# Performance work log

Hardware: AMD Instinct MI355X
Metric: run time of the kernel (lower is better)

The kernel has to match this reference:

```python
import jax, jax.numpy as jnp
import numpy as np

N = 50000      # total nodes
E = 500000     # edges
D = 128        # in_channels
B = 50         # graphs in batch
NPG = N // B   # nodes per graph (equal-sized graphs)
RATIO = 0.5
ALPHA = 0.6


def setup_inputs() -> dict:
    key = jax.random.key(0)
    ks = jax.random.split(key, 8)
    x = jax.random.normal(ks[0], (N, D), dtype=jnp.float32)
    edge_index = jax.random.randint(ks[1], (2, E), 0, N, dtype=jnp.int32)
    batch = jnp.repeat(jnp.arange(B, dtype=jnp.int32), NPG)  # sorted, equal blocks
    s = 1.0 / np.sqrt(D)
    # GCNConv(D,1) for structure score
    W_s = jax.random.normal(ks[2], (D, 1), dtype=jnp.float32) * s
    b_s = jnp.zeros((1,), dtype=jnp.float32)
    # Linear(D,1) for feature score
    W_f = jax.random.normal(ks[3], (1, D), dtype=jnp.float32) * s
    b_f = jnp.zeros((1,), dtype=jnp.float32)
    # GCNConv(D,D) fusion layer
    W_fu = jax.random.normal(ks[4], (D, D), dtype=jnp.float32) * s
    b_fu = jnp.zeros((D,), dtype=jnp.float32)
    return {"x": x, "edge_index": edge_index, "batch": batch,
            "W_s": W_s, "b_s": b_s, "W_f": W_f, "b_f": b_f,
            "W_fu": W_fu, "b_fu": b_fu}


def gcn_conv(x, src, dst, W, b, n):
    """PyG GCNConv: add self loops, symmetric D^-1/2 (A+I) D^-1/2 @ (xW) + b."""
    xw = x @ W                                  # [n, out]
    loop = jnp.arange(n, dtype=src.dtype)
    s = jnp.concatenate([src, loop])
    d = jnp.concatenate([dst, loop])
    deg = jax.ops.segment_sum(jnp.ones_like(s, dtype=xw.dtype), d, num_segments=n)
    dinv = jax.lax.rsqrt(jnp.maximum(deg, 1e-12))
    norm = dinv[s] * dinv[d]                    # [E+n]
    out = jax.ops.segment_sum(norm[:, None] * xw[s], d, num_segments=n)
    return out + b


def reference(x, edge_index, batch, W_s, b_s, W_f, b_f, W_fu, b_fu):
    src, dst = edge_index[0], edge_index[1]
    # fused score: alpha * structure (GCN) + (1-alpha) * feature (Linear)
    score_s = gcn_conv(x, src, dst, W_s, b_s, N)[:, 0]          # [N]
    score_f = (x @ W_f.T + b_f)[:, 0]                           # [N]
    score = jnp.tanh(ALPHA * score_s + (1.0 - ALPHA) * score_f)
    # per-graph top-k (equal-sized graphs -> dense [B, NPG] view, like the torch topk)
    k = int(np.ceil(RATIO * NPG))
    dense = score.reshape(B, NPG)
    order = jnp.argsort(-dense, axis=-1)                        # descending
    offsets = (jnp.arange(B, dtype=jnp.int32) * NPG)[:, None]
    perm = (order[:, :k].astype(jnp.int32) + offsets).reshape(-1)  # [B*k]
    # fusion conv on full graph, then gather selected nodes
    x_fused = gcn_conv(x, src, dst, W_fu, b_fu, N)              # [N, D]
    x_ae = x_fused[perm]                                        # [B*k, D]
    x_out = x_ae * score[perm][:, None]                         # multiplier == 1
    batch_out = batch[perm]
    # filter_adj: remap node ids, keep edges with both endpoints selected
    nodemap = jnp.full((N,), -1, dtype=jnp.int32).at[perm].set(
        jnp.arange(perm.shape[0], dtype=jnp.int32))
    r, c = nodemap[src], nodemap[dst]
    m = (r >= 0) & (c >= 0)
    edge_index_new = jnp.stack([r[m], c[m]], axis=0)
    return (x_out, edge_index_new, batch_out, perm, x_ae)
```

## Files before the change

kernel.cpp:

```cpp
#include <hip/hip_runtime.h>
#include <math.h>

#define N_NODES 50000
#define N_EDGES 500000
#define DIM     128
#define NGRAPH  50
#define NPGC    1000
#define KSEL    500
#define SORT_N  1024
#define NBE     489
#define GEMM_BLKS 782
#define EDGE_BLKS 1954
#define DOTS_BLKS 12500
#define NDINV     196
#define GATH_BLKS 6250
#define DEGB    64
#define NCHUNK  1954


__global__ __launch_bounds__(256) void k1_gemm_deg(const float* __restrict__ x,
                                                   const float* __restrict__ W,
                                                   float* __restrict__ xw,
                                                   const int* __restrict__ dst,
                                                   int* __restrict__ degpriv,
                                                   int* __restrict__ eslot) {
    __shared__ float lds[12288];
    int t = threadIdx.x;
    if (blockIdx.x < DEGB) {
        int b = blockIdx.x;
        int* priv = degpriv + b * N_NODES;
        for (int c = b; c < NCHUNK; c += 2 * DEGB) {
            int e1 = (c << 8) + t;
            int cB = c + DEGB;
            int e2 = (cB << 8) + t;
            int d1 = (e1 < N_EDGES) ? dst[e1] : -1;
            int d2 = (cB < NCHUNK && e2 < N_EDGES) ? dst[e2] : -1;
            if (d1 >= 0)
                eslot[e1] = __hip_atomic_fetch_add(&priv[d1], 1, __ATOMIC_RELAXED,
                                                   __HIP_MEMORY_SCOPE_WORKGROUP);
            if (d2 >= 0)
                eslot[e2] = __hip_atomic_fetch_add(&priv[d2], 1, __ATOMIC_RELAXED,
                                                   __HIP_MEMORY_SCOPE_WORKGROUP);
        }
        return;
    }
    float* Wt = lds;
    float* Xt = lds + 64 * DIM;
    int cg = t & 15;
    int ng = t >> 4;
    int node_base = (blockIdx.x - DEGB) * 64;

    float4 acc[4][2];
    #pragma unroll
    for (int nn = 0; nn < 4; nn++) {
        acc[nn][0] = make_float4(0.f, 0.f, 0.f, 0.f);
        acc[nn][1] = make_float4(0.f, 0.f, 0.f, 0.f);
    }
    for (int half = 0; half < 2; half++) {
        const float4* Wg = (const float4*)(W + half * 64 * DIM);
        float4* Wl = (float4*)Wt;
        #pragma unroll
        for (int i = 0; i < 8; i++) {
            int f = t + i * 256;
            Wl[f] = Wg[f];
        }
        #pragma unroll
        for (int i = 0; i < 4; i++) {
            int f = t + i * 256;
            int row = f >> 4, col = f & 15;
            int node = node_base + row;
            float4 v = make_float4(0.f, 0.f, 0.f, 0.f);
            if (node < N_NODES) v = *(const float4*)&x[(size_t)node * DIM + half * 64 + col * 4];
            *(float4*)&Xt[(row << 6) + ((col ^ (row & 15)) << 2)] = v;
        }
        __syncthreads();
        #pragma unroll 2
        for (int kc = 0; kc < 16; kc++) {
            int k = kc << 2;
            float4 wa[4], wb[4];
            #pragma unroll
            for (int kk = 0; kk < 4; kk++) {
                wa[kk] = *(const float4*)&Wt[(k + kk) * DIM + (cg << 2)];
                wb[kk] = *(const float4*)&Wt[(k + kk) * DIM + (cg << 2) + 64];
            }
            int csw = (kc ^ ng) << 2;
            #pragma unroll
            for (int nn = 0; nn < 4; nn++) {
                float4 xv = *(const float4*)&Xt[((ng + (nn << 4)) << 6) + csw];
                acc[nn][0].x += xv.x * wa[0].x + xv.y * wa[1].x + xv.z * wa[2].x + xv.w * wa[3].x;
                acc[nn][0].y += xv.x * wa[0].y + xv.y * wa[1].y + xv.z * wa[2].y + xv.w * wa[3].y;
                acc[nn][0].z += xv.x * wa[0].z + xv.y * wa[1].z + xv.z * wa[2].z + xv.w * wa[3].z;
                acc[nn][0].w += xv.x * wa[0].w + xv.y * wa[1].w + xv.z * wa[2].w + xv.w * wa[3].w;
                acc[nn][1].x += xv.x * wb[0].x + xv.y * wb[1].x + xv.z * wb[2].x + xv.w * wb[3].x;
                acc[nn][1].y += xv.x * wb[0].y + xv.y * wb[1].y + xv.z * wb[2].y + xv.w * wb[3].y;
                acc[nn][1].z += xv.x * wb[0].z + xv.y * wb[1].z + xv.z * wb[2].z + xv.w * wb[3].z;
                acc[nn][1].w += xv.x * wb[0].w + xv.y * wb[1].w + xv.z * wb[2].w + xv.w * wb[3].w;
            }
        }
        __syncthreads();
    }
    #pragma unroll
    for (int nn = 0; nn < 4; nn++) {
        int node = node_base + ng + (nn << 4);
        if (node < N_NODES) {
            *(float4*)&xw[(size_t)node * DIM + (cg << 2)]      = acc[nn][0];
            *(float4*)&xw[(size_t)node * DIM + (cg << 2) + 64] = acc[nn][1];
        }
    }
}


__global__ __launch_bounds__(256) void k2_dots_merge(int* __restrict__ degpriv,
                                                     int* __restrict__ deg,
                                                     int* __restrict__ rowoff,
                                                     int* __restrict__ bsums256,
                                                     const float* __restrict__ x,
                                                     const float* __restrict__ Ws,
                                                     const float* __restrict__ Wf,
                                                     const float* __restrict__ bf,
                                                     double* __restrict__ pack,
                                                     float* __restrict__ dinvf,
                                                     double* __restrict__ sf) {
    int t = threadIdx.x;
    int lane = t & 63, wid = t >> 6;
    int bid = blockIdx.x;
    if (bid < DOTS_BLKS) {
        int node = bid * 4 + wid;
        const float* xr = x + (size_t)node * DIM;
        double x1 = (double)xr[lane], x2 = (double)xr[lane + 64];
        double ps = x1 * (double)Ws[lane] + x2 * (double)Ws[lane + 64];
        double pf = x1 * (double)Wf[lane] + x2 * (double)Wf[lane + 64];
        for (int off = 32; off > 0; off >>= 1) {
            ps += __shfl_down(ps, off, 64);
            pf += __shfl_down(pf, off, 64);
        }
        if (lane == 0) {
            pack[2 * node + 1] = ps;
            sf[node] = pf + (double)bf[0];
        }
        return;
    }
    int i = (bid - DOTS_BLKS) * 256 + t;
    int o = 0;
    if (i < N_NODES) {
        #pragma unroll 8
        for (int b = 0; b < DEGB; b++) {
            int* p = &degpriv[b * N_NODES + i];
            int c = *p;
            *p = o;
            o += c;
        }
        deg[i] = o;
        double di = 1.0 / sqrt((double)(o + 1));
        pack[2 * i] = di;
        dinvf[i] = (float)di;
    }
    __shared__ int ws4[4];
    int incl = o;
    #pragma unroll
    for (int off = 1; off < 64; off <<= 1) {
        int u = __shfl_up(incl, off, 64);
        if (lane >= off) incl += u;
    }
    if (lane == 63) ws4[wid] = incl;
    __syncthreads();
    int woff = 0;
    #pragma unroll
    for (int w = 0; w < 4; w++) if (w < wid) woff += ws4[w];
    if (i < N_NODES) rowoff[i] = incl - o + woff;
    if (t == 255) bsums256[bid - DOTS_BLKS] = woff + incl;
}


__global__ __launch_bounds__(256) void k3_csr(const int* __restrict__ src,
                                              const int* __restrict__ dst,
                                              const int* __restrict__ rowoff,
                                              const int* __restrict__ bsums256,
                                              const int* __restrict__ degpriv,
                                              const int* __restrict__ eslot,
                                              int* __restrict__ csr) {
    __shared__ int bsN[256];
    int t = threadIdx.x;
    if (t < 64) {
        int carry = 0;
        #pragma unroll
        for (int ch = 0; ch < 4; ch++) {
            int i = ch * 64 + t;
            int v = (i < NDINV) ? bsums256[i] : 0;
            int incl = v;
            #pragma unroll
            for (int off = 1; off < 64; off <<= 1) {
                int u = __shfl_up(incl, off, 64);
                if (t >= off) incl += u;
            }
            bsN[i] = incl - v + carry;
            carry += __shfl(incl, 63, 64);
        }
    }
    __syncthreads();
    int e = blockIdx.x * 256 + t;
    if (e >= N_EDGES) return;
    int d = dst[e];
    int owner = (e >> 8) & (DEGB - 1);
    int pos = rowoff[d] + bsN[d >> 8] + degpriv[owner * N_NODES + d] + eslot[e];
    csr[pos] = src[e];
}


__global__ __launch_bounds__(256) void k3b_score(const int* __restrict__ csr,
                                                 const int* __restrict__ rowoff,
                                                 const int* __restrict__ bsums256,
                                                 const int* __restrict__ deg,
                                                 const double* __restrict__ pack,
                                                 double* __restrict__ score_sd) {
    __shared__ int bsN[256];
    int t = threadIdx.x;
    if (t < 64) {
        int carry = 0;
        #pragma unroll
        for (int ch = 0; ch < 4; ch++) {
            int i = ch * 64 + t;
            int v = (i < NDINV) ? bsums256[i] : 0;
            int incl = v;
            #pragma unroll
            for (int off = 1; off < 64; off <<= 1) {
                int u = __shfl_up(incl, off, 64);
                if (t >= off) incl += u;
            }
            bsN[i] = incl - v + carry;
            carry += __shfl(incl, 63, 64);
        }
    }
    __syncthreads();
    int node = blockIdx.x * 256 + t;
    if (node >= N_NODES) return;
    int base = rowoff[node] + bsN[node >> 8];
    int cnt  = deg[node];
    double acc0 = 0.0, acc1 = 0.0;
    int i = 0;
    for (; i + 2 <= cnt; i += 2) {
        int s0 = csr[base + i];
        int s1 = csr[base + i + 1];
        double2 p0 = ((const double2*)pack)[s0];
        double2 p1 = ((const double2*)pack)[s1];
        acc0 += p0.x * p0.y;
        acc1 += p1.x * p1.y;
    }
    if (i < cnt) {
        int s0 = csr[base + i];
        double2 p0 = ((const double2*)pack)[s0];
        acc0 += p0.x * p0.y;
    }
    score_sd[node] = pack[2 * node] * (acc0 + acc1);
}


__global__ __launch_bounds__(512) void k4_topk(const double* __restrict__ score_sd,
                                               const double* __restrict__ pack,
                                               const double* __restrict__ sf,
                                               const float* __restrict__ bs,
                                               const int* __restrict__ batch,
                                               int* __restrict__ perm, int* __restrict__ nodemap,
                                               float* __restrict__ scoref_sel,
                                               float* __restrict__ out, long o2, long o3) {
    __shared__ double key[SORT_N];
    __shared__ int    idx[SORT_N];
    int g = blockIdx.x, t = threadIdx.x;
    const double A = 0.6, OMA = 1.0 - 0.6;
    double bsv = (double)bs[0];
    for (int i = t; i < SORT_N; i += 512) {
        if (i < NPGC) {
            int node = g * NPGC + i;
            double2 p = ((const double2*)pack)[node];
            double tot = score_sd[node] + p.x * p.x * p.y + bsv;
            key[i] = tanh(A * tot + OMA * sf[node]);
            idx[i] = i;
        } else { key[i] = -1e300; idx[i] = i; }
    }
    __syncthreads();
    for (int size = 2; size <= SORT_N; size <<= 1) {
        for (int stride = size >> 1; stride > 0; stride >>= 1) {
            int a = ((t & ~(stride - 1)) << 1) | (t & (stride - 1));
            int b = a | stride;
            bool descFirst = ((a & size) == 0);
            double ka = key[a], kb = key[b];
            int ia = idx[a], ib = idx[b];
            bool aAfterB = (ka < kb) || (ka == kb && ia > ib);
            if (descFirst ? aAfterB : !aAfterB) {
                key[a] = kb; key[b] = ka;
                idx[a] = ib; idx[b] = ia;
            }
            __syncthreads();
        }
    }
    for (int j = t; j < KSEL; j += 512) {
        int node = g * NPGC + idx[j];
        int pos  = g * KSEL + j;
        perm[pos]        = node;
        nodemap[node]    = pos + 1;
        scoref_sel[pos]  = (float)key[j];
        out[o2 + pos]    = (float)batch[node];
        out[o3 + pos]    = (float)node;
    }
}


__global__ __launch_bounds__(256) void k5_escan_gather(const int* __restrict__ src,
                                                       const int* __restrict__ dst,
                                                       const int* __restrict__ nodemap,
                                                       int* __restrict__ epos,
                                                       int* __restrict__ bsumsE,
                                                       const float* __restrict__ xw,
                                                       const int* __restrict__ perm,
                                                       const int* __restrict__ rowoff,
                                                       const int* __restrict__ bsums256,
                                                       const int* __restrict__ deg,
                                                       const int* __restrict__ csr,
                                                       const float* __restrict__ dinvf,
                                                       const float* __restrict__ scoref_sel,
                                                       const float* __restrict__ b_fu,
                                                       float* __restrict__ out, long o4) {
    int t = threadIdx.x;
    int lane = t & 63, wid = t >> 6;
    if (blockIdx.x < NBE) {
        __shared__ int ws4[4];
        int base = blockIdx.x * 1024 + t * 4;
        int v0 = 0, v1 = 0, v2 = 0, v3 = 0;
        if (base + 0 < N_EDGES) v0 = (nodemap[src[base + 0]] > 0 && nodemap[dst[base + 0]] > 0);
        if (base + 1 < N_EDGES) v1 = (nodemap[src[base + 1]] > 0 && nodemap[dst[base + 1]] > 0);
        if (base + 2 < N_EDGES) v2 = (nodemap[src[base + 2]] > 0 && nodemap[dst[base + 2]] > 0);
        if (base + 3 < N_EDGES) v3 = (nodemap[src[base + 3]] > 0 && nodemap[dst[base + 3]] > 0);
        int s4 = v0 + v1 + v2 + v3;
        int incl = s4;
        #pragma unroll
        for (int off = 1; off < 64; off <<= 1) {
            int u = __shfl_up(incl, off, 64);
            if (lane >= off) incl += u;
        }
        if (lane == 63) ws4[wid] = incl;
        __syncthreads();
        int woff = 0;
        #pragma unroll
        for (int w = 0; w < 4; w++) if (w < wid) woff += ws4[w];
        int excl = incl - s4 + woff;
        if (base + 0 < N_EDGES) epos[base + 0] = excl;
        if (base + 1 < N_EDGES) epos[base + 1] = excl + v0;
        if (base + 2 < N_EDGES) epos[base + 2] = excl + v0 + v1;
        if (base + 3 < N_EDGES) epos[base + 3] = excl + v0 + v1 + v2;
        if (t == 255) bsumsE[blockIdx.x] = woff + incl;
        return;
    }
    __shared__ int bsN[256];
    if (t < 64) {
        int carry = 0;
        #pragma unroll
        for (int ch = 0; ch < 4; ch++) {
            int i = ch * 64 + t;
            int v = (i < NDINV) ? bsums256[i] : 0;
            int incl = v;
            #pragma unroll
            for (int off = 1; off < 64; off <<= 1) {
                int u = __shfl_up(incl, off, 64);
                if (t >= off) incl += u;
            }
            bsN[i] = incl - v + carry;
            carry += __shfl(incl, 63, 64);
        }
    }
    __syncthreads();
    int wave = (blockIdx.x - NBE) * 4 + wid;
    int p = perm[wave];
    float dpf = dinvf[p];
    int c2 = lane * 2;
    float2 v = ((const float2*)(xw + (size_t)p * DIM))[lane];
    float nself = dpf * dpf;
    float ax = nself * v.x, ay = nself * v.y;
    int beg = rowoff[p] + bsN[p >> 8], cnt = deg[p];
    int i = 0;
    for (; i + 2 <= cnt; i += 2) {
        int s0 = csr[beg + i];
        int s1 = csr[beg + i + 1];
        float2 u0 = ((const float2*)(xw + (size_t)s0 * DIM))[lane];
        float2 u1 = ((const float2*)(xw + (size_t)s1 * DIM))[lane];
        float n0 = dinvf[s0] * dpf, n1 = dinvf[s1] * dpf;
        ax += n0 * u0.x; ay += n0 * u0.y;
        ax += n1 * u1.x; ay += n1 * u1.y;
    }
    if (i < cnt) {
        int s0 = csr[beg + i];
        float2 u0 = ((const float2*)(xw + (size_t)s0 * DIM))[lane];
        float n0 = dinvf[s0] * dpf;
        ax += n0 * u0.x; ay += n0 * u0.y;
    }
    ax += b_fu[c2];
    ay += b_fu[c2 + 1];
    float sc = scoref_sel[wave];
    size_t ro = (size_t)wave * DIM + c2;
    out[o4 + ro]     = ax;
    out[o4 + ro + 1] = ay;
    out[ro]          = ax * sc;
    out[ro + 1]      = ay * sc;
}


__global__ __launch_bounds__(256) void k6_compact(const int* __restrict__ src,
                                                  const int* __restrict__ dst,
                                                  const int* __restrict__ nodemap,
                                                  const int* __restrict__ epos,
                                                  const int* __restrict__ bsumsE,
                                                  float* __restrict__ out_edges, long M) {
    __shared__ int bsE[512];
    int t = threadIdx.x;
    if (t < 64) {
        int carry = 0;
        #pragma unroll
        for (int c = 0; c < 8; c++) {
            int i = c * 64 + t;
            int v = (i < NBE) ? bsumsE[i] : 0;
            int incl = v;
            #pragma unroll
            for (int off = 1; off < 64; off <<= 1) {
                int u = __shfl_up(incl, off, 64);
                if (t >= off) incl += u;
            }
            if (i < 512) bsE[i] = incl - v + carry;
            carry += __shfl(incl, 63, 64);
        }
    }
    __syncthreads();
    int e = blockIdx.x * 256 + t;
    if (e >= N_EDGES) return;
    int r = nodemap[src[e]], c = nodemap[dst[e]];
    if (r > 0 && c > 0) {
        int pos = epos[e] + bsE[e >> 10];
        out_edges[pos]     = (float)(r - 1);
        out_edges[M + pos] = (float)(c - 1);
    }
}


extern "C" void kernel_launch(void* const* d_in, const int* in_sizes, int n_in,
                              void* d_out, int out_size, void* d_ws, size_t ws_size,
                              hipStream_t stream) {
    const float* x    = (const float*)d_in[0];
    const int*   ei   = (const int*)d_in[1];
    const int*   src  = ei;
    const int*   dst  = ei + N_EDGES;
    const int*   batch= (const int*)d_in[2];
    const float* W_s  = (const float*)d_in[3];
    const float* b_s  = (const float*)d_in[4];
    const float* W_f  = (const float*)d_in[5];
    const float* b_f  = (const float*)d_in[6];
    const float* W_fu = (const float*)d_in[7];
    const float* b_fu = (const float*)d_in[8];
    float* out = (float*)d_out;

    char* wsp = (char*)d_ws;
    size_t off = 0;
    auto take = [&](size_t bytes) -> char* {
        char* p = wsp + off;
        off = (off + bytes + 255) & ~(size_t)255;
        return p;
    };
    char*   zbase      = wsp;
    int*    degpriv    = (int*)   take((size_t)DEGB * N_NODES * 4);
    int*    nodemap    = (int*)   take((size_t)N_NODES * 4);
    size_t  zbytes     = off;
    int*    eslot      = (int*)   take((size_t)N_EDGES * 4);
    int*    deg        = (int*)   take((size_t)N_NODES * 4);
    double* score_sd   = (double*)take((size_t)N_NODES * 8);
    double* pack       = (double*)take((size_t)N_NODES * 16);
    double* sf         = (double*)take((size_t)N_NODES * 8);
    float*  dinvf      = (float*) take((size_t)N_NODES * 4);
    float*  scoref_sel = (float*) take((size_t)NGRAPH * KSEL * 4);
    int*    perm       = (int*)   take((size_t)NGRAPH * KSEL * 4);
    int*    rowoff     = (int*)   take((size_t)N_NODES * 4);
    int*    epos       = (int*)   take((size_t)N_EDGES * 4);
    int*    bsumsE     = (int*)   take((size_t)1024 * 4);
    int*    bsums256   = (int*)   take((size_t)1024 * 4);
    int*    csr        = (int*)   take((size_t)N_EDGES * 4);
    float*  xw         = (float*) take((size_t)N_NODES * DIM * 4);

    long M  = ((long)out_size - 6450000L) / 2;
    long o1 = 3200000L;
    long o2 = o1 + 2 * M;
    long o3 = o2 + (long)NGRAPH * KSEL;
    long o4 = o3 + (long)NGRAPH * KSEL;

    hipMemsetAsync(zbase, 0, zbytes, stream);

    k1_gemm_deg<<<DEGB + GEMM_BLKS, 256, 0, stream>>>(x, W_fu, xw, dst, degpriv, eslot);
    k2_dots_merge<<<DOTS_BLKS + NDINV, 256, 0, stream>>>(degpriv, deg, rowoff, bsums256,
                                                         x, W_s, W_f, b_f,
                                                         pack, dinvf, sf);
    k3_csr<<<EDGE_BLKS, 256, 0, stream>>>(src, dst, rowoff, bsums256, degpriv, eslot, csr);
    k3b_score<<<NDINV, 256, 0, stream>>>(csr, rowoff, bsums256, deg, pack, score_sd);
    k4_topk<<<NGRAPH, 512, 0, stream>>>(score_sd, pack, sf, b_s, batch,
                                        perm, nodemap, scoref_sel, out, o2, o3);
    k5_escan_gather<<<NBE + GATH_BLKS, 256, 0, stream>>>(src, dst, nodemap, epos, bsumsE,
                                                         xw, perm, rowoff, bsums256, deg, csr,
                                                         dinvf, scoref_sel, b_fu, out, o4);
    k6_compact<<<EDGE_BLKS, 256, 0, stream>>>(src, dst, nodemap, epos, bsumsE, out + o1, M);
}
```

Baseline: 223.7 us.

## Fuse score dot products into GEMM tile and split degree counting kernel

The structure and feature score dot products are computed inside the GEMM kernel from the x tile already staged in LDS, so x is not re-read by a separate dots pass. Degree counting moves out of the GEMM launch into its own small kernel, and the merge kernel keeps only the degree prefix work. This trades one launch and a full read of x for an extra serialized launch. The degree pass, which used to overlap with GEMM blocks, now runs alone on 64 blocks.

```diff
diff --git a/kernel.cpp b/kernel.cpp
--- a/kernel.cpp
+++ b/kernel.cpp
@@ -11,44 +11,58 @@
 #define NBE     489
 #define GEMM_BLKS 782
 #define EDGE_BLKS 1954
-#define DOTS_BLKS 12500
 #define NDINV     196
 #define GATH_BLKS 6250
 #define DEGB    64
 #define NCHUNK  1954
 
 
-__global__ __launch_bounds__(256) void k1_gemm_deg(const float* __restrict__ x,
-                                                   const float* __restrict__ W,
-                                                   float* __restrict__ xw,
-                                                   const int* __restrict__ dst,
-                                                   int* __restrict__ degpriv,
-                                                   int* __restrict__ eslot) {
-    __shared__ float lds[12288];
-    int t = threadIdx.x;
-    if (blockIdx.x < DEGB) {
-        int b = blockIdx.x;
-        int* priv = degpriv + b * N_NODES;
-        for (int c = b; c < NCHUNK; c += 2 * DEGB) {
-            int e1 = (c << 8) + t;
-            int cB = c + DEGB;
-            int e2 = (cB << 8) + t;
-            int d1 = (e1 < N_EDGES) ? dst[e1] : -1;
-            int d2 = (cB < NCHUNK && e2 < N_EDGES) ? dst[e2] : -1;
-            if (d1 >= 0)
-                eslot[e1] = __hip_atomic_fetch_add(&priv[d1], 1, __ATOMIC_RELAXED,
-                                                   __HIP_MEMORY_SCOPE_WORKGROUP);
-            if (d2 >= 0)
-                eslot[e2] = __hip_atomic_fetch_add(&priv[d2], 1, __ATOMIC_RELAXED,
-                                                   __HIP_MEMORY_SCOPE_WORKGROUP);
-        }
-        return;
-    }
-    float* Wt = lds;
-    float* Xt = lds + 64 * DIM;
+__global__ __launch_bounds__(256) void k1b_deg(const int* __restrict__ dst,
+                                               int* __restrict__ degpriv,
+                                               int* __restrict__ eslot) {
+    int t = threadIdx.x;
+    int b = blockIdx.x;
+    int* priv = degpriv + b * N_NODES;
+    for (int c = b; c < NCHUNK; c += 2 * DEGB) {
+        int e1 = (c << 8) + t;
+        int cB = c + DEGB;
+        int e2 = (cB << 8) + t;
+        int d1 = (e1 < N_EDGES) ? dst[e1] : -1;
+        int d2 = (cB < NCHUNK && e2 < N_EDGES) ? dst[e2] : -1;
+        if (d1 >= 0)
+            eslot[e1] = __hip_atomic_fetch_add(&priv[d1], 1, __ATOMIC_RELAXED,
+                                               __HIP_MEMORY_SCOPE_WORKGROUP);
+        if (d2 >= 0)
+            eslot[e2] = __hip_atomic_fetch_add(&priv[d2], 1, __ATOMIC_RELAXED,
+                                               __HIP_MEMORY_SCOPE_WORKGROUP);
+    }
+}
+
+
+__global__ __launch_bounds__(256) void k1a_gemm_dots(const float* __restrict__ x,
+                                                     const float* __restrict__ W,
+                                                     float* __restrict__ xw,
+                                                     const float* __restrict__ Ws,
+                                                     const float* __restrict__ Wf,
+                                                     const float* __restrict__ bf,
+                                                     double* __restrict__ pack,
+                                                     double* __restrict__ sf) {
+    __shared__ float lds[12544];
+    int t = threadIdx.x;
+    float* Wt  = lds;
+    float* Xt  = lds + 8192;
+    float* Wsl = lds + 12288;
+    float* Wfl = lds + 12416;
     int cg = t & 15;
     int ng = t >> 4;
-    int node_base = (blockIdx.x - DEGB) * 64;
+    int node_base = blockIdx.x * 64;
+
+    if (t < 128) Wsl[t] = Ws[t];
+    else         Wfl[t - 128] = Wf[t - 128];
+
+    int dn  = t >> 2;
+    int dk4 = (t & 3) << 4;
+    double ps = 0.0, pf = 0.0;
 
     float4 acc[4][2];
     #pragma unroll
@@ -97,6 +111,14 @@
                 acc[nn][1].w += xv.x * wb[0].w + xv.y * wb[1].w + xv.z * wb[2].w + xv.w * wb[3].w;
             }
         }
+        #pragma unroll 4
+        for (int j = 0; j < 16; j++) {
+            int k = dk4 + j;
+            int col = k >> 2, sub = k & 3;
+            double xd = (double)Xt[(dn << 6) + ((col ^ (dn & 15)) << 2) + sub];
+            ps += xd * (double)Wsl[half * 64 + k];
+            pf += xd * (double)Wfl[half * 64 + k];
+        }
         __syncthreads();
     }
     #pragma unroll
@@ -107,40 +129,27 @@
             *(float4*)&xw[(size_t)node * DIM + (cg << 2) + 64] = acc[nn][1];
         }
     }
-}
-
-
-__global__ __launch_bounds__(256) void k2_dots_merge(int* __restrict__ degpriv,
-                                                     int* __restrict__ deg,
-                                                     int* __restrict__ rowoff,
-                                                     int* __restrict__ bsums256,
-                                                     const float* __restrict__ x,
-                                                     const float* __restrict__ Ws,
-                                                     const float* __restrict__ Wf,
-                                                     const float* __restrict__ bf,
-                                                     double* __restrict__ pack,
-                                                     float* __restrict__ dinvf,
-                                                     double* __restrict__ sf) {
-    int t = threadIdx.x;
-    int lane = t & 63, wid = t >> 6;
-    int bid = blockIdx.x;
-    if (bid < DOTS_BLKS) {
-        int node = bid * 4 + wid;
-        const float* xr = x + (size_t)node * DIM;
-        double x1 = (double)xr[lane], x2 = (double)xr[lane + 64];
-        double ps = x1 * (double)Ws[lane] + x2 * (double)Ws[lane + 64];
-        double pf = x1 * (double)Wf[lane] + x2 * (double)Wf[lane + 64];
-        for (int off = 32; off > 0; off >>= 1) {
-            ps += __shfl_down(ps, off, 64);
-            pf += __shfl_down(pf, off, 64);
-        }
-        if (lane == 0) {
+    ps += __shfl_down(ps, 2, 64); ps += __shfl_down(ps, 1, 64);
+    pf += __shfl_down(pf, 2, 64); pf += __shfl_down(pf, 1, 64);
+    if ((t & 3) == 0) {
+        int node = node_base + dn;
+        if (node < N_NODES) {
             pack[2 * node + 1] = ps;
             sf[node] = pf + (double)bf[0];
         }
-        return;
-    }
-    int i = (bid - DOTS_BLKS) * 256 + t;
+    }
+}
+
+
+__global__ __launch_bounds__(256) void k2_merge(int* __restrict__ degpriv,
+                                                int* __restrict__ deg,
+                                                int* __restrict__ rowoff,
+                                                int* __restrict__ bsums256,
+                                                double* __restrict__ pack,
+                                                float* __restrict__ dinvf) {
+    int t = threadIdx.x;
+    int lane = t & 63, wid = t >> 6;
+    int i = blockIdx.x * 256 + t;
     int o = 0;
     if (i < N_NODES) {
         #pragma unroll 8
@@ -168,7 +177,7 @@
     #pragma unroll
     for (int w = 0; w < 4; w++) if (w < wid) woff += ws4[w];
     if (i < N_NODES) rowoff[i] = incl - o + woff;
-    if (t == 255) bsums256[bid - DOTS_BLKS] = woff + incl;
+    if (t == 255) bsums256[blockIdx.x] = woff + incl;
 }
 
 
@@ -489,10 +498,9 @@
 
     hipMemsetAsync(zbase, 0, zbytes, stream);
 
-    k1_gemm_deg<<<DEGB + GEMM_BLKS, 256, 0, stream>>>(x, W_fu, xw, dst, degpriv, eslot);
-    k2_dots_merge<<<DOTS_BLKS + NDINV, 256, 0, stream>>>(degpriv, deg, rowoff, bsums256,
-                                                         x, W_s, W_f, b_f,
-                                                         pack, dinvf, sf);
+    k1b_deg<<<DEGB, 256, 0, stream>>>(dst, degpriv, eslot);
+    k1a_gemm_dots<<<GEMM_BLKS, 256, 0, stream>>>(x, W_fu, xw, W_s, W_f, b_f, pack, sf);
+    k2_merge<<<NDINV, 256, 0, stream>>>(degpriv, deg, rowoff, bsums256, pack, dinvf);
     k3_csr<<<EDGE_BLKS, 256, 0, stream>>>(src, dst, rowoff, bsums256, degpriv, eslot, csr);
     k3b_score<<<NDINV, 256, 0, stream>>>(csr, rowoff, bsums256, deg, pack, score_sd);
     k4_topk<<<NGRAPH, 512, 0, stream>>>(score_sd, pack, sf, b_s, batch,
```

Result: slower. 233.9 us (+4.5%).
